# Performance work log

Measured on AMD Instinct MI355X. Metric: run time of the kernel, lower is better.

Reference implementation:

```python
import jax, jax.numpy as jnp
import numpy as np

DIM = 1536
DSTATE = 16


def setup_inputs() -> dict:
    key = jax.random.key(0)
    ks = jax.random.split(key, 8)
    batch, dim, seqlen, dstate = 4, DIM, 4096, DSTATE
    u = jax.random.normal(ks[0], (batch, dim, seqlen), dtype=jnp.float32)
    delta = jax.random.uniform(ks[1], (batch, dim, seqlen), dtype=jnp.float32)
    B = jax.random.normal(ks[2], (batch, dstate, seqlen), dtype=jnp.float32)
    C = jax.random.normal(ks[3], (batch, dstate, seqlen), dtype=jnp.float32)
    A = -jnp.exp(jax.random.normal(ks[4], (dim, dstate), dtype=jnp.float32))
    D = jax.random.normal(ks[5], (dim,), dtype=jnp.float32)
    delta_bias = jax.random.normal(ks[6], (dim,), dtype=jnp.float32)
    return {"u": u, "delta": delta, "B": B, "C": C, "A": A, "D": D, "delta_bias": delta_bias}


def _selective_scan(u, delta, B, C, A, D, delta_bias):
    # u, delta: [b, d, s]; B, C: [b, n, s]; A: [d, n]; D, delta_bias: [d]
    dt = jax.nn.softplus(delta + delta_bias[None, :, None])  # [b, d, s]
    # scan over time: carry x [b, d, n]
    dt_s = jnp.moveaxis(dt, 2, 0)   # [s, b, d]
    u_s = jnp.moveaxis(u, 2, 0)     # [s, b, d]
    B_s = jnp.moveaxis(B, 2, 0)     # [s, b, n]
    C_s = jnp.moveaxis(C, 2, 0)     # [s, b, n]

    def step(x, inp):
        dt_t, u_t, B_t, C_t = inp  # [b,d], [b,d], [b,n], [b,n]
        dA = jnp.exp(dt_t[..., None] * A[None])           # [b, d, n]
        dBu = (dt_t * u_t)[..., None] * B_t[:, None, :]   # [b, d, n]
        x = dA * x + dBu
        y = jnp.einsum('bdn,bn->bd', x, C_t) + D[None] * u_t
        return x, y

    b, d, s = u.shape
    n = A.shape[1]
    x0 = jnp.zeros((b, d, n), dtype=jnp.float32)
    _, ys = jax.lax.scan(step, x0, (dt_s, u_s, B_s, C_s))  # ys: [s, b, d]
    return jnp.moveaxis(ys, 0, 2)  # [b, d, s]


def reference(u, delta, B, C, A, D, delta_bias):
    return _selective_scan(u, delta, B, C, A, D, delta_bias)
```

## Files before the change

kernel.cpp:

```cpp
#include <hip/hip_runtime.h>

#define BATCH 4
#define DIM   1536
#define SEQ   4096
#define NST   16
#define NCH   32
#define CLEN  128
#define NCHAN (BATCH*DIM)
#define T     16
#define LSTR  17

#define LOG2E 1.4426950408889634f

__device__ __forceinline__ float softplus_f(float z) {
    return (z > 20.f) ? z : __logf(1.f + __expf(z));
}

__device__ __forceinline__ float exp2_hw(float z) {
    return __builtin_amdgcn_exp2f(z);
}

__global__ __launch_bounds__(256) void ssm_phaseA(
    const float* __restrict__ u, const float* __restrict__ delta,
    const float* __restrict__ Bm, const float* __restrict__ A,
    const float* __restrict__ dbias,
    float* __restrict__ sumdt_out, float* __restrict__ S_out)
{
    __shared__ float lu[256 * LSTR];
    __shared__ float ld[256 * LSTR];
    __shared__ float lB[T * NST];

    const int tid = threadIdx.x;
    const int ch  = blockIdx.x * 256 + tid;
    const int d   = ch % DIM;
    const int bb  = (blockIdx.x * 256) / DIM;
    const int k   = blockIdx.y;
    const int s0  = k * CLEN;

    float Arow2[NST];
    const float* Ap = A + d * NST;
#pragma unroll
    for (int n = 0; n < NST; n++) Arow2[n] = Ap[n] * LOG2E;
    const float bias = dbias[d];

    const size_t gbase = (size_t)(blockIdx.x * 256) * SEQ + s0;

    float S[NST];
#pragma unroll
    for (int n = 0; n < NST; n++) S[n] = 0.f;
    float sumdt = 0.f;

    for (int ss = 0; ss < CLEN; ss += T) {
        __syncthreads();
#pragma unroll
        for (int q = 0; q < 4; q++) {
            const int idx = tid + 256 * q;
            const int co  = idx >> 2;
            const int i4  = (idx & 3) << 2;
            const float4 uv = *(const float4*)(u     + gbase + (size_t)co * SEQ + ss + i4);
            const float4 dv = *(const float4*)(delta + gbase + (size_t)co * SEQ + ss + i4);
            float* lup = &lu[co * LSTR + i4];
            float* ldp = &ld[co * LSTR + i4];
            lup[0] = uv.x; lup[1] = uv.y; lup[2] = uv.z; lup[3] = uv.w;
            ldp[0] = dv.x; ldp[1] = dv.y; ldp[2] = dv.z; ldp[3] = dv.w;
        }
        {
            const int n = tid >> 4, i = tid & 15;
            lB[i * NST + n] = Bm[((size_t)(bb * NST + n)) * SEQ + s0 + ss + i];
        }
        __syncthreads();

        const float* lur = &lu[tid * LSTR];
        const float* ldr = &ld[tid * LSTR];
#pragma unroll
        for (int i = 0; i < T; i++) {
            const float uu  = lur[i];
            const float dt  = softplus_f(ldr[i] + bias);
            const float dtu = dt * uu;
            sumdt += dt;
            const float* bi = &lB[i * NST];
#pragma unroll
            for (int n = 0; n < NST; n++) {
                const float a = exp2_hw(dt * Arow2[n]);
                S[n] = fmaf(a, S[n], dtu * bi[n]);
            }
        }
    }

    const size_t base = ((size_t)k * NCHAN + ch) * NST;
#pragma unroll
    for (int n = 0; n < NST; n += 4)
        *(float4*)(S_out + base + n) = make_float4(S[n], S[n+1], S[n+2], S[n+3]);
    sumdt_out[(size_t)k * NCHAN + ch] = sumdt;
}

__global__ __launch_bounds__(256) void ssm_phaseB(
    const float* __restrict__ A, const float* __restrict__ sumdt,
    float* __restrict__ S)
{
    const int t  = blockIdx.x * 256 + threadIdx.x;
    const int n  = t & 15;
    const int ch = t >> 4;
    if (ch >= NCHAN) return;
    const int d = ch % DIM;
    const float An2 = A[d * NST + n] * LOG2E;
    float x = 0.f;
    for (int k = 0; k < NCH; k++) {
        const size_t idx = ((size_t)k * NCHAN + ch) * NST + n;
        const float s_old = S[idx];
        S[idx] = x;
        const float P = exp2_hw(An2 * sumdt[(size_t)k * NCHAN + ch]);
        x = fmaf(P, x, s_old);
    }
}

__global__ __launch_bounds__(256) void ssm_phaseC(
    const float* __restrict__ u, const float* __restrict__ delta,
    const float* __restrict__ Bm, const float* __restrict__ Cm,
    const float* __restrict__ A, const float* __restrict__ Dv,
    const float* __restrict__ dbias, const float* __restrict__ x0,
    float* __restrict__ y)
{
    __shared__ float lu[256 * LSTR];
    __shared__ float ld[256 * LSTR];
    __shared__ float ly[256 * LSTR];
    __shared__ float lB[T * NST];
    __shared__ float lC[T * NST];

    const int tid = threadIdx.x;
    const int ch  = blockIdx.x * 256 + tid;
    const int d   = ch % DIM;
    const int bb  = (blockIdx.x * 256) / DIM;
    const int k   = blockIdx.y;
    const int s0  = k * CLEN;

    float Arow2[NST];
    const float* Ap = A + d * NST;
#pragma unroll
    for (int n = 0; n < NST; n++) Arow2[n] = Ap[n] * LOG2E;
    const float bias = dbias[d];
    const float Dval = Dv[d];

    float x[NST];
    const size_t xbase = ((size_t)k * NCHAN + ch) * NST;
#pragma unroll
    for (int n = 0; n < NST; n += 4) {
        const float4 xv = *(const float4*)(x0 + xbase + n);
        x[n] = xv.x; x[n+1] = xv.y; x[n+2] = xv.z; x[n+3] = xv.w;
    }

    const size_t gbase = (size_t)(blockIdx.x * 256) * SEQ + s0;

    for (int ss = 0; ss < CLEN; ss += T) {
        __syncthreads();
#pragma unroll
        for (int q = 0; q < 4; q++) {
            const int idx = tid + 256 * q;
            const int co  = idx >> 2;
            const int i4  = (idx & 3) << 2;
            const float4 uv = *(const float4*)(u     + gbase + (size_t)co * SEQ + ss + i4);
            const float4 dv = *(const float4*)(delta + gbase + (size_t)co * SEQ + ss + i4);
            float* lup = &lu[co * LSTR + i4];
            float* ldp = &ld[co * LSTR + i4];
            lup[0] = uv.x; lup[1] = uv.y; lup[2] = uv.z; lup[3] = uv.w;
            ldp[0] = dv.x; ldp[1] = dv.y; ldp[2] = dv.z; ldp[3] = dv.w;
        }
        {
            const int n = tid >> 4, i = tid & 15;
            const size_t g = ((size_t)(bb * NST + n)) * SEQ + s0 + ss + i;
            lB[i * NST + n] = Bm[g];
            lC[i * NST + n] = Cm[g];
        }
        __syncthreads();

        const float* lur = &lu[tid * LSTR];
        const float* ldr = &ld[tid * LSTR];
        float*       lyw = &ly[tid * LSTR];
#pragma unroll
        for (int i = 0; i < T; i++) {
            const float uu  = lur[i];
            const float dt  = softplus_f(ldr[i] + bias);
            const float dtu = dt * uu;
            const float* bi = &lB[i * NST];
            const float* ci = &lC[i * NST];
            float acc = Dval * uu;
#pragma unroll
            for (int n = 0; n < NST; n++) {
                const float a = exp2_hw(dt * Arow2[n]);
                x[n] = fmaf(a, x[n], dtu * bi[n]);
                acc  = fmaf(x[n], ci[n], acc);
            }
            lyw[i] = acc;
        }
        __syncthreads();
#pragma unroll
        for (int q = 0; q < 4; q++) {
            const int idx = tid + 256 * q;
            const int co  = idx >> 2;
            const int i4  = (idx & 3) << 2;
            const float* lyr = &ly[co * LSTR + i4];
            *(float4*)(y + gbase + (size_t)co * SEQ + ss + i4) =
                make_float4(lyr[0], lyr[1], lyr[2], lyr[3]);
        }
    }
}

extern "C" void kernel_launch(void* const* d_in, const int* in_sizes, int n_in,
                              void* d_out, int out_size, void* d_ws, size_t ws_size,
                              hipStream_t stream)
{
    const float* u     = (const float*)d_in[0];
    const float* delta = (const float*)d_in[1];
    const float* Bm    = (const float*)d_in[2];
    const float* Cm    = (const float*)d_in[3];
    const float* A     = (const float*)d_in[4];
    const float* Dv    = (const float*)d_in[5];
    const float* dbias = (const float*)d_in[6];
    float* y = (float*)d_out;

    float* sumdt = (float*)d_ws;
    float* S     = sumdt + (size_t)NCHAN * NCH;

    const dim3 grid(NCHAN / 256, NCH);
    ssm_phaseA<<<grid, 256, 0, stream>>>(u, delta, Bm, A, dbias, sumdt, S);
    ssm_phaseB<<<(NCHAN * NST) / 256, 256, 0, stream>>>(A, sumdt, S);
    ssm_phaseC<<<grid, 256, 0, stream>>>(u, delta, Bm, Cm, A, Dv, dbias, S, y);
}
```

Before: 495.5 us.

## Use per-wavefront LDS staging with register prefetch and drop block barriers

```diff
diff --git a/kernel.cpp b/kernel.cpp
--- a/kernel.cpp
+++ b/kernel.cpp
@@ -9,41 +9,59 @@
 #define NCHAN (BATCH*DIM)
 #define T     16
 #define LSTR  17
+#define WLDS  (64*LSTR)
 
 #define LOG2E 1.4426950408889634f
 
 __device__ __forceinline__ float softplus_f(float z) {
     return (z > 20.f) ? z : __logf(1.f + __expf(z));
 }
-
 __device__ __forceinline__ float exp2_hw(float z) {
     return __builtin_amdgcn_exp2f(z);
 }
 
-__global__ __launch_bounds__(256) void ssm_phaseA(
+__global__ __launch_bounds__(256, 4) void ssm_phaseA(
     const float* __restrict__ u, const float* __restrict__ delta,
     const float* __restrict__ Bm, const float* __restrict__ A,
     const float* __restrict__ dbias,
     float* __restrict__ sumdt_out, float* __restrict__ S_out)
 {
-    __shared__ float lu[256 * LSTR];
-    __shared__ float ld[256 * LSTR];
-    __shared__ float lB[T * NST];
+    __shared__ float lu[4 * WLDS];
+    __shared__ float ld[4 * WLDS];
+    __shared__ float lB[4 * T * NST];
 
     const int tid = threadIdx.x;
+    const int w   = tid >> 6;
+    const int l   = tid & 63;
     const int ch  = blockIdx.x * 256 + tid;
     const int d   = ch % DIM;
     const int bb  = (blockIdx.x * 256) / DIM;
     const int k   = blockIdx.y;
     const int s0  = k * CLEN;
 
-    float Arow2[NST];
+    float* Lu = &lu[w * WLDS];
+    float* Ld = &ld[w * WLDS];
+    float* LB = &lB[w * T * NST];
+
+    float A2[NST];
     const float* Ap = A + d * NST;
 #pragma unroll
-    for (int n = 0; n < NST; n++) Arow2[n] = Ap[n] * LOG2E;
+    for (int n = 0; n < NST; n++) A2[n] = Ap[n] * LOG2E;
     const float bias = dbias[d];
 
-    const size_t gbase = (size_t)(blockIdx.x * 256) * SEQ + s0;
+    const int coB = l >> 2;
+    const int i4  = (l & 3) << 2;
+    const size_t rowbase = (size_t)(blockIdx.x * 256 + w * 64) * SEQ + s0;
+    const size_t bbase   = (size_t)(bb * NST + coB) * SEQ + s0;
+
+    float4 ru[4], rd[4], rb;
+#pragma unroll
+    for (int q = 0; q < 4; q++) {
+        const size_t g = rowbase + (size_t)(q * 16 + coB) * SEQ + i4;
+        ru[q] = *(const float4*)(u + g);
+        rd[q] = *(const float4*)(delta + g);
+    }
+    rb = *(const float4*)(Bm + bbase + i4);
 
     float S[NST];
 #pragma unroll
@@ -51,37 +69,40 @@
     float sumdt = 0.f;
 
     for (int ss = 0; ss < CLEN; ss += T) {
-        __syncthreads();
 #pragma unroll
         for (int q = 0; q < 4; q++) {
-            const int idx = tid + 256 * q;
-            const int co  = idx >> 2;
-            const int i4  = (idx & 3) << 2;
-            const float4 uv = *(const float4*)(u     + gbase + (size_t)co * SEQ + ss + i4);
-            const float4 dv = *(const float4*)(delta + gbase + (size_t)co * SEQ + ss + i4);
-            float* lup = &lu[co * LSTR + i4];
-            float* ldp = &ld[co * LSTR + i4];
-            lup[0] = uv.x; lup[1] = uv.y; lup[2] = uv.z; lup[3] = uv.w;
-            ldp[0] = dv.x; ldp[1] = dv.y; ldp[2] = dv.z; ldp[3] = dv.w;
-        }
-        {
-            const int n = tid >> 4, i = tid & 15;
-            lB[i * NST + n] = Bm[((size_t)(bb * NST + n)) * SEQ + s0 + ss + i];
-        }
-        __syncthreads();
-
-        const float* lur = &lu[tid * LSTR];
-        const float* ldr = &ld[tid * LSTR];
+            float* pu = &Lu[(q * 16 + coB) * LSTR + i4];
+            float* pd = &Ld[(q * 16 + coB) * LSTR + i4];
+            pu[0] = ru[q].x; pu[1] = ru[q].y; pu[2] = ru[q].z; pu[3] = ru[q].w;
+            pd[0] = rd[q].x; pd[1] = rd[q].y; pd[2] = rd[q].z; pd[3] = rd[q].w;
+        }
+        LB[(i4 + 0) * NST + coB] = rb.x;
+        LB[(i4 + 1) * NST + coB] = rb.y;
+        LB[(i4 + 2) * NST + coB] = rb.z;
+        LB[(i4 + 3) * NST + coB] = rb.w;
+
+        if (ss + T < CLEN) {
+#pragma unroll
+            for (int q = 0; q < 4; q++) {
+                const size_t g = rowbase + (size_t)(q * 16 + coB) * SEQ + (ss + T) + i4;
+                ru[q] = *(const float4*)(u + g);
+                rd[q] = *(const float4*)(delta + g);
+            }
+            rb = *(const float4*)(Bm + bbase + (ss + T) + i4);
+        }
+
+        const float* lur = &Lu[l * LSTR];
+        const float* ldr = &Ld[l * LSTR];
 #pragma unroll
         for (int i = 0; i < T; i++) {
             const float uu  = lur[i];
             const float dt  = softplus_f(ldr[i] + bias);
             const float dtu = dt * uu;
             sumdt += dt;
-            const float* bi = &lB[i * NST];
+            const float* bi = &LB[i * NST];
 #pragma unroll
             for (int n = 0; n < NST; n++) {
-                const float a = exp2_hw(dt * Arow2[n]);
+                const float a = exp2_hw(dt * A2[n]);
                 S[n] = fmaf(a, S[n], dtu * bi[n]);
             }
         }
@@ -114,30 +135,36 @@
     }
 }
 
-__global__ __launch_bounds__(256) void ssm_phaseC(
+__global__ __launch_bounds__(256, 4) void ssm_phaseC(
     const float* __restrict__ u, const float* __restrict__ delta,
     const float* __restrict__ Bm, const float* __restrict__ Cm,
     const float* __restrict__ A, const float* __restrict__ Dv,
     const float* __restrict__ dbias, const float* __restrict__ x0,
     float* __restrict__ y)
 {
-    __shared__ float lu[256 * LSTR];
-    __shared__ float ld[256 * LSTR];
-    __shared__ float ly[256 * LSTR];
-    __shared__ float lB[T * NST];
-    __shared__ float lC[T * NST];
+    __shared__ float lu[4 * WLDS];
+    __shared__ float ld[4 * WLDS];
+    __shared__ float lB[4 * T * NST];
+    __shared__ float lC[4 * T * NST];
 
     const int tid = threadIdx.x;
+    const int w   = tid >> 6;
+    const int l   = tid & 63;
     const int ch  = blockIdx.x * 256 + tid;
     const int d   = ch % DIM;
     const int bb  = (blockIdx.x * 256) / DIM;
     const int k   = blockIdx.y;
     const int s0  = k * CLEN;
 
-    float Arow2[NST];
+    float* Lu = &lu[w * WLDS];
+    float* Ld = &ld[w * WLDS];
+    float* LB = &lB[w * T * NST];
+    float* LC = &lC[w * T * NST];
+
+    float A2[NST];
     const float* Ap = A + d * NST;
 #pragma unroll
-    for (int n = 0; n < NST; n++) Arow2[n] = Ap[n] * LOG2E;
+    for (int n = 0; n < NST; n++) A2[n] = Ap[n] * LOG2E;
     const float bias = dbias[d];
     const float Dval = Dv[d];
 
@@ -149,58 +176,73 @@
         x[n] = xv.x; x[n+1] = xv.y; x[n+2] = xv.z; x[n+3] = xv.w;
     }
 
-    const size_t gbase = (size_t)(blockIdx.x * 256) * SEQ + s0;
+    const int coB = l >> 2;
+    const int i4  = (l & 3) << 2;
+    const size_t rowbase = (size_t)(blockIdx.x * 256 + w * 64) * SEQ + s0;
+    const size_t bbase   = (size_t)(bb * NST + coB) * SEQ + s0;
+
+    float4 ru[4], rd[4], rb, rc;
+#pragma unroll
+    for (int q = 0; q < 4; q++) {
+        const size_t g = rowbase + (size_t)(q * 16 + coB) * SEQ + i4;
+        ru[q] = *(const float4*)(u + g);
+        rd[q] = *(const float4*)(delta + g);
+    }
+    rb = *(const float4*)(Bm + bbase + i4);
+    rc = *(const float4*)(Cm + bbase + i4);
 
     for (int ss = 0; ss < CLEN; ss += T) {
-        __syncthreads();
 #pragma unroll
         for (int q = 0; q < 4; q++) {
-            const int idx = tid + 256 * q;
-            const int co  = idx >> 2;
-            const int i4  = (idx & 3) << 2;
-            const float4 uv = *(const float4*)(u     + gbase + (size_t)co * SEQ + ss + i4);
-            const float4 dv = *(const float4*)(delta + gbase + (size_t)co * SEQ + ss + i4);
-            float* lup = &lu[co * LSTR + i4];
-            float* ldp = &ld[co * LSTR + i4];
-            lup[0] = uv.x; lup[1] = uv.y; lup[2] = uv.z; lup[3] = uv.w;
-            ldp[0] = dv.x; ldp[1] = dv.y; ldp[2] = dv.z; ldp[3] = dv.w;
-        }
-        {
-            const int n = tid >> 4, i = tid & 15;
-            const size_t g = ((size_t)(bb * NST + n)) * SEQ + s0 + ss + i;
-            lB[i * NST + n] = Bm[g];
-            lC[i * NST + n] = Cm[g];
-        }
-        __syncthreads();
-
-        const float* lur = &lu[tid * LSTR];
-        const float* ldr = &ld[tid * LSTR];
-        float*       lyw = &ly[tid * LSTR];
+            float* pu = &Lu[(q * 16 + coB) * LSTR + i4];
+            float* pd = &Ld[(q * 16 + coB) * LSTR + i4];
+            pu[0] = ru[q].x; pu[1] = ru[q].y; pu[2] = ru[q].z; pu[3] = ru[q].w;
+            pd[0] = rd[q].x; pd[1] = rd[q].y; pd[2] = rd[q].z; pd[3] = rd[q].w;
+        }
+        LB[(i4 + 0) * NST + coB] = rb.x;
+        LB[(i4 + 1) * NST + coB] = rb.y;
+        LB[(i4 + 2) * NST + coB] = rb.z;
+        LB[(i4 + 3) * NST + coB] = rb.w;
+        LC[(i4 + 0) * NST + coB] = rc.x;
+        LC[(i4 + 1) * NST + coB] = rc.y;
+        LC[(i4 + 2) * NST + coB] = rc.z;
+        LC[(i4 + 3) * NST + coB] = rc.w;
+
+        if (ss + T < CLEN) {
+#pragma unroll
+            for (int q = 0; q < 4; q++) {
+                const size_t g = rowbase + (size_t)(q * 16 + coB) * SEQ + (ss + T) + i4;
+                ru[q] = *(const float4*)(u + g);
+                rd[q] = *(const float4*)(delta + g);
+            }
+            rb = *(const float4*)(Bm + bbase + (ss + T) + i4);
+            rc = *(const float4*)(Cm + bbase + (ss + T) + i4);
+        }
+
+        float* lur = &Lu[l * LSTR];
+        const float* ldr = &Ld[l * LSTR];
 #pragma unroll
         for (int i = 0; i < T; i++) {
             const float uu  = lur[i];
             const float dt  = softplus_f(ldr[i] + bias);
             const float dtu = dt * uu;
-            const float* bi = &lB[i * NST];
-            const float* ci = &lC[i * NST];
+            const float* bi = &LB[i * NST];
+            const float* ci = &LC[i * NST];
             float acc = Dval * uu;
 #pragma unroll
             for (int n = 0; n < NST; n++) {
-                const float a = exp2_hw(dt * Arow2[n]);
+                const float a = exp2_hw(dt * A2[n]);
                 x[n] = fmaf(a, x[n], dtu * bi[n]);
                 acc  = fmaf(x[n], ci[n], acc);
             }
-            lyw[i] = acc;
-        }
-        __syncthreads();
+            lur[i] = acc;
+        }
+
 #pragma unroll
         for (int q = 0; q < 4; q++) {
-            const int idx = tid + 256 * q;
-            const int co  = idx >> 2;
-            const int i4  = (idx & 3) << 2;
-            const float* lyr = &ly[co * LSTR + i4];
-            *(float4*)(y + gbase + (size_t)co * SEQ + ss + i4) =
-                make_float4(lyr[0], lyr[1], lyr[2], lyr[3]);
+            const float* pr = &Lu[(q * 16 + coB) * LSTR + i4];
+            *(float4*)(y + rowbase + (size_t)(q * 16 + coB) * SEQ + ss + i4) =
+                make_float4(pr[0], pr[1], pr[2], pr[3]);
         }
     }
 }
```

Measured after the change: 494.0 us. No clear change (-0.3%).
